# Optimization experiments

Measured on AMD Instinct MI355X. Metric: run time of the kernel, lower is better.

Reference implementation:

```python
import jax, jax.numpy as jnp
import numpy as np

V, D, E, K = 8192, 128, 262144, 512

def _sqrtm_psd(A):
    # symmetric PSD matrix square root via eigendecomposition
    w, v = jnp.linalg.eigh(A)
    w = jnp.clip(w, 0.0)
    return (v * jnp.sqrt(w)) @ v.T


def setup_inputs() -> dict:
    key = jax.random.key(0)
    k1, k2, k3, k4 = jax.random.split(key, 4)
    inputs = jax.random.normal(k1, (V, D), dtype=jnp.float32) * 0.1
    # targets must be SPD (it is passed through sqrtm as a covariance)
    A = jax.random.normal(k2, (K, K), dtype=jnp.float32) / np.sqrt(K)
    targets = A @ A.T + 0.1 * jnp.eye(K, dtype=jnp.float32)
    edge_index = jax.random.randint(k3, (2, E), 0, V, dtype=jnp.int32)
    pmat = jax.random.normal(k4, (K, V), dtype=jnp.float32) / np.sqrt(V)
    return {"inputs": inputs, "targets": targets, "edge_index": edge_index, "pmat": pmat}


def reference(inputs, targets, edge_index, pmat):
    n = inputs.shape[0]
    i, j = edge_index[0], edge_index[1]
    # per-edge squared distance -> exp weight (vectorized gather-compute)
    d = jnp.sum((inputs[i] - inputs[j]) ** 2, axis=-1)  # [E]
    w = jnp.exp(-d)
    # W starts as identity (self loops give exp(0)=1, same as eye); symmetric scatter
    W = jnp.eye(n, dtype=inputs.dtype)
    W = W.at[i, j].set(w).at[j, i].set(w)
    deg = W.sum(axis=1)
    L = jnp.diag(deg) - W
    k = pmat.shape[0]
    L_adj = pmat @ L @ pmat.T + 1e-05 * jnp.eye(k, dtype=inputs.dtype)
    S1 = jnp.linalg.inv(L_adj)
    S0 = targets.astype(jnp.float32)
    S0_sqrt = _sqrtm_psd(S0)
    S_ = _sqrtm_psd(S0_sqrt @ S1 @ S0_sqrt)
    return jnp.trace(S1) + jnp.trace(S0) - 2.0 * jnp.trace(S_)
```

## Files before the change

kernel.cpp:

```cpp
#include <hip/hip_runtime.h>
#include <math.h>

#define VN 8192
#define DN 128
#define EN 262144
#define KD 512
#define KK (KD*KD)

#define S_SS_LADJ 0
#define S_INV_C1  1
#define S_SS_S0   2
#define S_INV_C0  3
#define S_QRT_C0  4
#define S_SS_G    5
#define S_INV_CG  6
#define S_QRT_CG  7
#define S_TR_X    8
#define S_TR_S0   9
#define S_TR_YG   10

typedef __attribute__((ext_vector_type(8))) __bf16 bf16x8;
typedef __attribute__((ext_vector_type(4))) float f32x4;

static __device__ __forceinline__ float waveReduceAdd(float v) {
#pragma unroll
  for (int o = 32; o; o >>= 1) v += __shfl_xor(v, o);
  return v;
}

static __device__ __forceinline__ ushort f2b(float f) {
  unsigned x = __float_as_uint(f);
  unsigned r = (x + 0x7fffu + ((x >> 16) & 1u)) >> 16;
  return (ushort)r;
}
static __device__ __forceinline__ float b2f(ushort u) {
  return __uint_as_float((unsigned)u << 16);
}


__global__ __launch_bounds__(256) void transpose_k(const float* __restrict__ in,
                                                   float* __restrict__ out) {
  __shared__ float s[32][33];
  int tx = threadIdx.x & 31, ty = threadIdx.x >> 5;
  int v0 = blockIdx.x * 32, k0 = blockIdx.y * 32;
  for (int r = ty; r < 32; r += 8) s[r][tx] = in[(size_t)(k0 + r) * VN + v0 + tx];
  __syncthreads();
  for (int r = ty; r < 32; r += 8) out[(size_t)(v0 + r) * KD + k0 + tx] = s[tx][r];
}

__global__ __launch_bounds__(256) void count_k(const float* __restrict__ x,
                                               const int* __restrict__ ei,
                                               int* __restrict__ ea, int* __restrict__ eb,
                                               float* __restrict__ ew,
                                               int* __restrict__ cnt,
                                               unsigned int* __restrict__ bitmap) {
  int e = (int)(((unsigned)blockIdx.x * 256u + threadIdx.x) >> 6);
  int lane = threadIdx.x & 63;
  if (e >= EN) return;
  int i = ei[e], j = ei[EN + e];
  int a = i < j ? i : j;
  int b = i < j ? j : i;
  int ok = 0;
  if (lane == 0) {
    if (i != j) {
      unsigned key = (unsigned)a * (unsigned)VN + (unsigned)b;
      unsigned m = 1u << (key & 31u);
      unsigned old = atomicOr(bitmap + (key >> 5), m);
      ok = (old & m) ? 0 : 1;
    }
  }
  ok = __shfl(ok, 0);
  if (!ok) { if (lane == 0) ea[e] = -1; return; }
  float d0 = x[a * DN + lane]      - x[b * DN + lane];
  float d1 = x[a * DN + 64 + lane] - x[b * DN + 64 + lane];
  float s = d0 * d0 + d1 * d1;
  s = waveReduceAdd(s);
  if (lane == 0) {
    ea[e] = a; eb[e] = b; ew[e] = expf(-s);
    atomicAdd(cnt + a, 1);
    atomicAdd(cnt + b, 1);
  }
}

__global__ __launch_bounds__(1024) void scan_k(const int* __restrict__ cnt,
                                               int* __restrict__ rowptr,
                                               int* __restrict__ cursor) {
  __shared__ int sd[1024];
  __shared__ int carry;
  int tid = threadIdx.x;
  if (tid == 0) { carry = 0; rowptr[0] = 0; }
  __syncthreads();
  for (int c = 0; c < VN / 1024; ++c) {
    int v = c * 1024 + tid;
    int xv = cnt[v];
    sd[tid] = xv;
    __syncthreads();
    for (int off = 1; off < 1024; off <<= 1) {
      int t = (tid >= off) ? sd[tid - off] : 0;
      __syncthreads();
      sd[tid] += t;
      __syncthreads();
    }
    int incl = sd[tid];
    int base = carry;
    rowptr[v + 1] = base + incl;
    cursor[v] = base + incl - xv;
    __syncthreads();
    if (tid == 1023) carry = base + incl;
    __syncthreads();
  }
}

__global__ __launch_bounds__(256) void fill_k(const int* __restrict__ ea, const int* __restrict__ eb,
                                              const float* __restrict__ ew,
                                              int* __restrict__ cursor,
                                              int* __restrict__ adjj, float* __restrict__ adjw) {
  int e = blockIdx.x * 256 + threadIdx.x;
  if (e >= EN) return;
  int a = ea[e];
  if (a < 0) return;
  int b = eb[e];
  float w = ew[e];
  int p = atomicAdd(cursor + a, 1); adjj[p] = b; adjw[p] = w;
  int q = atomicAdd(cursor + b, 1); adjj[q] = a; adjw[q] = w;
}

__global__ __launch_bounds__(512) void buildB_k(const float* __restrict__ pmatT,
                                                const int* __restrict__ rowptr,
                                                const int* __restrict__ adjj,
                                                const float* __restrict__ adjw,
                                                float* __restrict__ Bout) {
  int v = blockIdx.x;
  int k = threadIdx.x;
  int s = rowptr[v], e = rowptr[v + 1];
  float a0 = 0.f, a1 = 0.f, a2 = 0.f, a3 = 0.f, sw = 0.f;
  int p = s;
  for (; p + 4 <= e; p += 4) {
    int j0 = adjj[p], j1 = adjj[p + 1], j2 = adjj[p + 2], j3 = adjj[p + 3];
    float w0 = adjw[p], w1 = adjw[p + 1], w2 = adjw[p + 2], w3 = adjw[p + 3];
    a0 += w0 * pmatT[(size_t)j0 * KD + k];
    a1 += w1 * pmatT[(size_t)j1 * KD + k];
    a2 += w2 * pmatT[(size_t)j2 * KD + k];
    a3 += w3 * pmatT[(size_t)j3 * KD + k];
    sw += w0 + w1 + w2 + w3;
  }
  for (; p < e; ++p) {
    int jj = adjj[p];
    float w = adjw[p];
    a0 += w * pmatT[(size_t)jj * KD + k];
    sw += w;
  }
  Bout[(size_t)v * KD + k] = sw * pmatT[(size_t)v * KD + k] - (a0 + a1 + a2 + a3);
}

__global__ __launch_bounds__(256) void gemm_big_k(const float* __restrict__ A,
                                                  const float* __restrict__ B,
                                                  float* __restrict__ C) {
  __shared__ __align__(16) float As[32][34];
  __shared__ __align__(16) float Bs[32][34];
  int tid = threadIdx.x;
  int tx = tid & 15, ty = tid >> 4;
  int n0 = blockIdx.x * 32, m0 = blockIdx.y * 32;
  int kbase = blockIdx.z * (VN / 8);
  float a00 = 0.f, a01 = 0.f, a10 = 0.f, a11 = 0.f;
  for (int kt = kbase; kt < kbase + VN / 8; kt += 32) {
#pragma unroll
    for (int u = 0; u < 4; ++u) {
      int li = tid * 4 + u;
      int r = li >> 5, c = li & 31;
      As[c][r] = A[(size_t)(m0 + r) * VN + kt + c];
      Bs[r][c] = B[(size_t)(kt + r) * KD + n0 + c];
    }
    __syncthreads();
#pragma unroll
    for (int k = 0; k < 32; ++k) {
      float2 av = *(const float2*)&As[k][2 * ty];
      float2 bv = *(const float2*)&Bs[k][2 * tx];
      a00 += av.x * bv.x; a01 += av.x * bv.y;
      a10 += av.y * bv.x; a11 += av.y * bv.y;
    }
    __syncthreads();
  }
  int m = m0 + 2 * ty, n = n0 + 2 * tx;
  atomicAdd(&C[m * KD + n], a00);
  atomicAdd(&C[m * KD + n + 1], a01);
  atomicAdd(&C[(m + 1) * KD + n], a10);
  atomicAdd(&C[(m + 1) * KD + n + 1], a11);
}


static __device__ __forceinline__ void g32_body(const float* __restrict__ A,
                                                const float* __restrict__ B,
                                                const float* __restrict__ Dm,
                                                float* __restrict__ C,
                                                float alpha, float beta) {
  __shared__ __align__(16) float As[32][34];
  __shared__ __align__(16) float Bs[32][34];
  int tid = threadIdx.x;
  int tx = tid & 15, ty = tid >> 4;
  int n0 = blockIdx.x * 32, m0 = blockIdx.y * 32;
  float a00 = 0.f, a01 = 0.f, a10 = 0.f, a11 = 0.f;
  for (int kt = 0; kt < KD; kt += 32) {
#pragma unroll
    for (int u = 0; u < 4; ++u) {
      int li = tid * 4 + u;
      int r = li >> 5, c = li & 31;
      As[c][r] = A[(m0 + r) * KD + kt + c];
      Bs[r][c] = B[(kt + r) * KD + n0 + c];
    }
    __syncthreads();
#pragma unroll
    for (int k = 0; k < 32; ++k) {
      float2 av = *(const float2*)&As[k][2 * ty];
      float2 bv = *(const float2*)&Bs[k][2 * tx];
      a00 += av.x * bv.x; a01 += av.x * bv.y;
      a10 += av.y * bv.x; a11 += av.y * bv.y;
    }
    __syncthreads();
  }
  int m = m0 + 2 * ty, n = n0 + 2 * tx;
  float d00 = 0.f, d01 = 0.f, d10 = 0.f, d11 = 0.f;
  if (beta != 0.0f) {
    d00 = Dm[m * KD + n];       d01 = Dm[m * KD + n + 1];
    d10 = Dm[(m + 1) * KD + n]; d11 = Dm[(m + 1) * KD + n + 1];
  }
  C[m * KD + n]           = alpha * a00 + beta * d00;
  C[m * KD + n + 1]       = alpha * a01 + beta * d01;
  C[(m + 1) * KD + n]     = alpha * a10 + beta * d10;
  C[(m + 1) * KD + n + 1] = alpha * a11 + beta * d11;
}

__global__ __launch_bounds__(256) void gemm_kk(const float* __restrict__ A,
                                               const float* __restrict__ B,
                                               const float* __restrict__ Dm,
                                               float* __restrict__ C,
                                               float alpha, float beta) {
  g32_body(A, B, Dm, C, alpha, beta);
}

__global__ __launch_bounds__(256) void gemm_dual32(const float* A0, const float* B0,
                                                   const float* D0, float* C0,
                                                   const float* A1, const float* B1,
                                                   const float* D1, float* C1,
                                                   float alpha, float beta) {
  if (blockIdx.z == 0) g32_body(A0, B0, D0, C0, alpha, beta);
  else                 g32_body(A1, B1, D1, C1, alpha, beta);
}


struct SmemT { ushort a[2][64][40]; ushort b[2][64][40]; };

static __device__ __forceinline__ void mgemm_s(SmemT* sm,
    const float* Asl, const float* Bsl, const float* Dsl, float* Csl,
    float alpha, float beta, int wsplit) {
  const ushort* Ah = (const ushort*)(Asl + KK);
  const ushort* Al = Ah + KK;
  const ushort* Bh = (const ushort*)(Bsl + KK);
  const ushort* Bl = Bh + KK;
  int tid = threadIdx.x;
  int lane = tid & 63, wave = tid >> 6;
  int wr = wave >> 1, wc = wave & 1;
  int fr = lane & 15, fq = lane >> 4;
  int m0 = blockIdx.y * 64, n0 = blockIdx.x * 64;
  int sr = tid >> 2, skc = (tid & 3) * 8;
  f32x4 acc[2][2] = {};
  for (int kt = 0; kt < KD; kt += 32) {
    *(uint4*)&sm->a[0][sr][skc] = *(const uint4*)&Ah[(size_t)(m0 + sr) * KD + kt + skc];
    *(uint4*)&sm->a[1][sr][skc] = *(const uint4*)&Al[(size_t)(m0 + sr) * KD + kt + skc];
    *(uint4*)&sm->b[0][sr][skc] = *(const uint4*)&Bh[(size_t)(n0 + sr) * KD + kt + skc];
    *(uint4*)&sm->b[1][sr][skc] = *(const uint4*)&Bl[(size_t)(n0 + sr) * KD + kt + skc];
    __syncthreads();
    bf16x8 ah[2], al[2], bh[2], bl[2];
#pragma unroll
    for (int m = 0; m < 2; ++m) {
      ah[m] = *(const bf16x8*)&sm->a[0][wr * 32 + m * 16 + fr][fq * 8];
      al[m] = *(const bf16x8*)&sm->a[1][wr * 32 + m * 16 + fr][fq * 8];
    }
#pragma unroll
    for (int n = 0; n < 2; ++n) {
      bh[n] = *(const bf16x8*)&sm->b[0][wc * 32 + n * 16 + fr][fq * 8];
      bl[n] = *(const bf16x8*)&sm->b[1][wc * 32 + n * 16 + fr][fq * 8];
    }
#pragma unroll
    for (int m = 0; m < 2; ++m)
#pragma unroll
      for (int n = 0; n < 2; ++n) {
        acc[m][n] = __builtin_amdgcn_mfma_f32_16x16x32_bf16(ah[m], bh[n], acc[m][n], 0, 0, 0);
        acc[m][n] = __builtin_amdgcn_mfma_f32_16x16x32_bf16(ah[m], bl[n], acc[m][n], 0, 0, 0);
        acc[m][n] = __builtin_amdgcn_mfma_f32_16x16x32_bf16(al[m], bh[n], acc[m][n], 0, 0, 0);
      }
    __syncthreads();
  }
  ushort* Ch = (ushort*)(Csl + KK);
  ushort* Cl = Ch + KK;
#pragma unroll
  for (int m = 0; m < 2; ++m)
#pragma unroll
    for (int n = 0; n < 2; ++n) {
      int col = n0 + wc * 32 + n * 16 + fr;
#pragma unroll
      for (int j = 0; j < 4; ++j) {
        int row = m0 + wr * 32 + m * 16 + fq * 4 + j;
        float v = alpha * acc[m][n][j];
        if (beta != 0.f) v += beta * Dsl[row * KD + col];
        Csl[row * KD + col] = v;
        if (wsplit) {
          ushort h = f2b(v);
          Ch[row * KD + col] = h;
          Cl[row * KD + col] = f2b(v - b2f(h));
        }
      }
    }
}

__global__ __launch_bounds__(256) void bc3_k(const float* Za, const float* Ya, float* Pm,
                                             const float* Xa, const float* Ra,
                                             float* Xb, float* Rb) {
  __shared__ SmemT sm;
  int z = blockIdx.z;
  if (z == 0)      mgemm_s(&sm, Za, Ya, nullptr, Pm, 1.f, 0.f, 1);
  else if (z == 1) mgemm_s(&sm, Xa, Ra, Xa, Xb, 1.f, 1.f, 1);
  else             mgemm_s(&sm, Ra, Ra, nullptr, Rb, 1.f, 0.f, 1);
}

__global__ __launch_bounds__(256) void yz2_k(const float* Ya, const float* Za, const float* Pm,
                                             float* Yb, float* Zb) {
  __shared__ SmemT sm;
  if (blockIdx.z == 0) mgemm_s(&sm, Ya, Pm, Ya, Yb, -0.5f, 1.5f, 1);
  else                 mgemm_s(&sm, Pm, Za, Za, Zb, -0.5f, 1.5f, 1);
}

__global__ __launch_bounds__(256) void pm1_k(const float* Za, const float* Ya, float* Pm) {
  __shared__ SmemT sm;
  mgemm_s(&sm, Za, Ya, nullptr, Pm, 1.f, 0.f, 1);
}


__global__ __launch_bounds__(256) void sumsq_k(const float* __restrict__ A, int n,
                                               float* __restrict__ slot) {
  float s = 0.f;
  for (int i = blockIdx.x * 256 + threadIdx.x; i < n; i += gridDim.x * 256) {
    float v = A[i];
    s += v * v;
  }
  __shared__ float p[4];
  s = waveReduceAdd(s);
  if ((threadIdx.x & 63) == 0) p[threadIdx.x >> 6] = s;
  __syncthreads();
  if (threadIdx.x == 0) atomicAdd(slot, p[0] + p[1] + p[2] + p[3]);
}

__global__ __launch_bounds__(512) void trace_k(const float* __restrict__ A,
                                               float* __restrict__ slot) {
  float v = A[(size_t)threadIdx.x * KD + threadIdx.x];
  __shared__ float p[8];
  v = waveReduceAdd(v);
  if ((threadIdx.x & 63) == 0) p[threadIdx.x >> 6] = v;
  __syncthreads();
  if (threadIdx.x == 0) {
    float t = 0.f;
    for (int i = 0; i < 8; ++i) t += p[i];
    slot[0] = t;
  }
}

__global__ void derive_k(const float* __restrict__ in, float* __restrict__ o_rsqrt,
                         float* __restrict__ o_qroot) {
  float x = in[0];
  o_rsqrt[0] = 1.0f / sqrtf(x);
  if (o_qroot) o_qroot[0] = powf(x, 0.25f);
}

__global__ __launch_bounds__(256) void setid_const_k(float* __restrict__ C, float val) {
  int idx = blockIdx.x * 256 + threadIdx.x;
  int r = idx >> 9, c = idx & (KD - 1);
  C[idx] = (r == c) ? val : 0.0f;
}

__global__ __launch_bounds__(256) void initinv_split_k(const float* __restrict__ Ladj,
                                                       const float* __restrict__ s,
                                                       float* __restrict__ X,
                                                       float* __restrict__ R) {
  int idx = blockIdx.x * 256 + threadIdx.x;
  int r = idx >> 9, c = idx & (KD - 1);
  float cv = s[0];
  float id = (r == c) ? 1.f : 0.f;
  float xv = id * cv;
  float rv = id - cv * Ladj[idx];
  ushort* Xh = (ushort*)(X + KK); ushort* Xl = Xh + KK;
  ushort* Rh = (ushort*)(R + KK); ushort* Rl = Rh + KK;
  X[idx] = xv; ushort h = f2b(xv); Xh[idx] = h; Xl[idx] = f2b(xv - b2f(h));
  R[idx] = rv; h = f2b(rv);        Rh[idx] = h; Rl[idx] = f2b(rv - b2f(h));
}

__global__ __launch_bounds__(256) void setid_split_k(float* __restrict__ C, float val) {
  int idx = blockIdx.x * 256 + threadIdx.x;
  int r = idx >> 9, c = idx & (KD - 1);
  float v = (r == c) ? val : 0.0f;
  ushort* Chh = (ushort*)(C + KK); ushort* Cll = Chh + KK;
  C[idx] = v; ushort h = f2b(v); Chh[idx] = h; Cll[idx] = f2b(v - b2f(h));
}

__global__ __launch_bounds__(256) void scale_split_k(const float* __restrict__ A,
                                                     const float* __restrict__ s,
                                                     float* __restrict__ C) {
  int idx = blockIdx.x * 256 + threadIdx.x;
  float v = A[idx] * s[0];
  ushort* Chh = (ushort*)(C + KK); ushort* Cll = Chh + KK;
  C[idx] = v; ushort h = f2b(v); Chh[idx] = h; Cll[idx] = f2b(v - b2f(h));
}

__global__ __launch_bounds__(256) void scale32_k(const float* __restrict__ A,
                                                 const float* __restrict__ s,
                                                 float* __restrict__ C) {
  int idx = blockIdx.x * 256 + threadIdx.x;
  C[idx] = A[idx] * s[0];
}

__global__ __launch_bounds__(256) void sym_k(const float* __restrict__ G,
                                             float* __restrict__ Out) {
  int idx = blockIdx.x * 256 + threadIdx.x;
  int r = idx >> 9, c = idx & (KD - 1);
  Out[idx] = 0.5f * (G[idx] + G[c * KD + r]);
}

__global__ void final_k(const float* __restrict__ scal, float* __restrict__ out) {
  out[0] = scal[S_TR_X] + scal[S_TR_S0] - 2.0f * scal[S_QRT_CG] * scal[S_TR_YG];
}


extern "C" void kernel_launch(void* const* d_in, const int* in_sizes, int n_in,
                              void* d_out, int out_size, void* d_ws, size_t ws_size,
                              hipStream_t stream) {
  (void)in_sizes; (void)n_in; (void)out_size; (void)ws_size;
  const float* x    = (const float*)d_in[0];
  const float* S0   = (const float*)d_in[1];
  const int*   ei   = (const int*)d_in[2];
  const float* pmat = (const float*)d_in[3];
  float* out = (float*)d_out;
  char* ws = (char*)d_ws;
  const size_t MB = 1u << 20;
  const size_t SLOT = 2 * MB;

  unsigned* bitmap = (unsigned*)ws;
  float* pmatT = (float*)(ws + 8 * MB);
  float* Bm    = (float*)(ws + 24 * MB);
  float* Ladj  = (float*)(ws + 40 * MB);
  float* Gs    = (float*)(ws + 41 * MB);
  int*   ea     = (int*)(ws + 40 * MB);
  int*   eb     = (int*)(ws + 41 * MB);
  float* ew     = (float*)(ws + 42 * MB);
  int*   adjj   = (int*)(ws + 43 * MB);
  float* adjw   = (float*)(ws + 45 * MB);
  int*   cnt    = (int*)(ws + 47 * MB);
  int*   rowptr = (int*)(ws + 47 * MB + 64 * 1024);
  int*   cursor = (int*)(ws + 47 * MB + 128 * 1024);
  float* scal   = (float*)(ws + 47 * MB + 256 * 1024);
  float* SL[11];
  for (int i = 0; i < 11; ++i) SL[i] = (float*)(ws + (size_t)i * SLOT);
  float *Xa = SL[0], *Ra = SL[1], *Ya = SL[2], *Za = SL[3];
  float *Xb = SL[4], *Rb = SL[5], *Yb = SL[6], *Zb = SL[7];
  float *Pm = SL[8], *S0h = SL[9], *TMP = SL[10];

  hipMemsetAsync(bitmap, 0, (size_t)VN * VN / 8, stream);
  hipMemsetAsync(cnt, 0, (size_t)VN * 4, stream);
  hipMemsetAsync(scal, 0, 64 * 4, stream);

  transpose_k<<<dim3(VN / 32, KD / 32), 256, 0, stream>>>(pmat, pmatT);
  count_k<<<EN / 4, 256, 0, stream>>>(x, ei, ea, eb, ew, cnt, bitmap);
  scan_k<<<1, 1024, 0, stream>>>(cnt, rowptr, cursor);
  fill_k<<<EN / 256, 256, 0, stream>>>(ea, eb, ew, cursor, adjj, adjw);
  buildB_k<<<VN, 512, 0, stream>>>(pmatT, rowptr, adjj, adjw, Bm);
  setid_const_k<<<KK / 256, 256, 0, stream>>>(Ladj, 1e-5f);
  gemm_big_k<<<dim3(16, 16, 8), 256, 0, stream>>>(pmat, Bm, Ladj);

  sumsq_k<<<256, 256, 0, stream>>>(Ladj, KK, &scal[S_SS_LADJ]);
  derive_k<<<1, 1, 0, stream>>>(&scal[S_SS_LADJ], &scal[S_INV_C1], nullptr);
  initinv_split_k<<<KK / 256, 256, 0, stream>>>(Ladj, &scal[S_INV_C1], Xa, Ra);

  sumsq_k<<<256, 256, 0, stream>>>(S0, KK, &scal[S_SS_S0]);
  derive_k<<<1, 1, 0, stream>>>(&scal[S_SS_S0], &scal[S_INV_C0], &scal[S_QRT_C0]);
  scale_split_k<<<KK / 256, 256, 0, stream>>>(S0, &scal[S_INV_C0], Ya);
  setid_split_k<<<KK / 256, 256, 0, stream>>>(Za, 1.0f);

  for (int r = 0; r < 15; ++r) {
    bc3_k<<<dim3(8, 8, 3), 256, 0, stream>>>(Za, Ya, Pm, Xa, Ra, Xb, Rb);
    yz2_k<<<dim3(8, 8, 2), 256, 0, stream>>>(Ya, Za, Pm, Yb, Zb);
    float* t = Xa; Xa = Xb; Xb = t;
    t = Ra; Ra = Rb; Rb = t;
    t = Ya; Ya = Yb; Yb = t;
    t = Za; Za = Zb; Zb = t;
  }

  float* U32  = Xb;
  float* Xfin = Rb;
  gemm_kk<<<dim3(16, 16), 256, 0, stream>>>(Ladj, Xa, nullptr, U32, 1.0f, 0.0f);
  gemm_kk<<<dim3(16, 16), 256, 0, stream>>>(Xa, U32, Xa, Xfin, -1.0f, 2.0f);
  trace_k<<<1, 512, 0, stream>>>(Xfin, &scal[S_TR_X]);
  trace_k<<<1, 512, 0, stream>>>(S0, &scal[S_TR_S0]);

  gemm_kk<<<dim3(16, 16), 256, 0, stream>>>(Za, Ya, nullptr, Pm, 1.0f, 0.0f);
  gemm_kk<<<dim3(16, 16), 256, 0, stream>>>(Ya, Pm, Ya, Yb, -0.5f, 1.5f);
  scale32_k<<<KK / 256, 256, 0, stream>>>(Yb, &scal[S_QRT_C0], S0h);

  gemm_kk<<<dim3(16, 16), 256, 0, stream>>>(S0h, Xfin, nullptr, TMP, 1.0f, 0.0f);
  gemm_kk<<<dim3(16, 16), 256, 0, stream>>>(TMP, S0h, nullptr, Gs, 1.0f, 0.0f);
  sym_k<<<KK / 256, 256, 0, stream>>>(Gs, TMP);
  sumsq_k<<<256, 256, 0, stream>>>(TMP, KK, &scal[S_SS_G]);
  derive_k<<<1, 1, 0, stream>>>(&scal[S_SS_G], &scal[S_INV_CG], &scal[S_QRT_CG]);
  scale_split_k<<<KK / 256, 256, 0, stream>>>(TMP, &scal[S_INV_CG], Ya);
  setid_split_k<<<KK / 256, 256, 0, stream>>>(Za, 1.0f);
  for (int r = 0; r < 20; ++r) {
    pm1_k<<<dim3(8, 8, 1), 256, 0, stream>>>(Za, Ya, Pm);
    yz2_k<<<dim3(8, 8, 2), 256, 0, stream>>>(Ya, Za, Pm, Yb, Zb);
    float* t = Ya; Ya = Yb; Yb = t;
    t = Za; Za = Zb; Zb = t;
  }
  gemm_kk<<<dim3(16, 16), 256, 0, stream>>>(Za, Ya, nullptr, Pm, 1.0f, 0.0f);
  gemm_dual32<<<dim3(16, 16, 2), 256, 0, stream>>>(Ya, Pm, Ya, Yb,
                                                   Pm, Za, Za, Zb, -0.5f, 1.5f);
  gemm_kk<<<dim3(16, 16), 256, 0, stream>>>(Zb, Yb, nullptr, Pm, 1.0f, 0.0f);
  gemm_kk<<<dim3(16, 16), 256, 0, stream>>>(Yb, Pm, Yb, S0h, -0.5f, 1.5f);
  trace_k<<<1, 512, 0, stream>>>(S0h, &scal[S_TR_YG]);

  final_k<<<1, 1, 0, stream>>>(scal, out);
}
```

Measured before the change: 1.580 ms.

## Vectorize edge distance, enlarge big GEMM tiles, batch tail GEMMs and traces

The edge kernel now uses 16 lanes per edge with float4 loads and a 16-lane shuffle reduction instead of a full wave per edge. The split-K projection GEMM moves from 32x32 to 64x64 output tiles with 4x4 register blocking, float4 loads and fewer atomics. Independent post-iteration GEMM pairs and the two trace reductions are merged into dual launches to cut kernel launch count. The cost is more registers in the GEMM and fewer blocks in flight.

New measurement: 1.466 ms. 7.2% less time.

```diff
diff --git a/kernel.cpp b/kernel.cpp
--- a/kernel.cpp
+++ b/kernel.cpp
@@ -54,14 +54,15 @@
                                                float* __restrict__ ew,
                                                int* __restrict__ cnt,
                                                unsigned int* __restrict__ bitmap) {
-  int e = (int)(((unsigned)blockIdx.x * 256u + threadIdx.x) >> 6);
+  int e = (int)(((unsigned)blockIdx.x * 256u + threadIdx.x) >> 4);
   int lane = threadIdx.x & 63;
+  int sl = lane & 15;
   if (e >= EN) return;
   int i = ei[e], j = ei[EN + e];
   int a = i < j ? i : j;
   int b = i < j ? j : i;
   int ok = 0;
-  if (lane == 0) {
+  if (sl == 0) {
     if (i != j) {
       unsigned key = (unsigned)a * (unsigned)VN + (unsigned)b;
       unsigned m = 1u << (key & 31u);
@@ -69,13 +70,17 @@
       ok = (old & m) ? 0 : 1;
     }
   }
-  ok = __shfl(ok, 0);
-  if (!ok) { if (lane == 0) ea[e] = -1; return; }
-  float d0 = x[a * DN + lane]      - x[b * DN + lane];
-  float d1 = x[a * DN + 64 + lane] - x[b * DN + 64 + lane];
-  float s = d0 * d0 + d1 * d1;
-  s = waveReduceAdd(s);
-  if (lane == 0) {
+  ok = __shfl(ok, lane & 48);
+  if (!ok) { if (sl == 0) ea[e] = -1; return; }
+  const float4* xa = (const float4*)&x[(size_t)a * DN + sl * 8];
+  const float4* xb = (const float4*)&x[(size_t)b * DN + sl * 8];
+  float4 a0 = xa[0], a1 = xa[1], b0 = xb[0], b1 = xb[1];
+  float d0 = a0.x - b0.x, d1 = a0.y - b0.y, d2 = a0.z - b0.z, d3 = a0.w - b0.w;
+  float d4 = a1.x - b1.x, d5 = a1.y - b1.y, d6 = a1.z - b1.z, d7 = a1.w - b1.w;
+  float s = d0*d0 + d1*d1 + d2*d2 + d3*d3 + d4*d4 + d5*d5 + d6*d6 + d7*d7;
+#pragma unroll
+  for (int o = 8; o; o >>= 1) s += __shfl_xor(s, o);
+  if (sl == 0) {
     ea[e] = a; eb[e] = b; ew[e] = expf(-s);
     atomicAdd(cnt + a, 1);
     atomicAdd(cnt + b, 1);
@@ -156,36 +161,42 @@
 __global__ __launch_bounds__(256) void gemm_big_k(const float* __restrict__ A,
                                                   const float* __restrict__ B,
                                                   float* __restrict__ C) {
-  __shared__ __align__(16) float As[32][34];
-  __shared__ __align__(16) float Bs[32][34];
+  __shared__ __align__(16) float As[32][68];
+  __shared__ __align__(16) float Bs[32][68];
   int tid = threadIdx.x;
   int tx = tid & 15, ty = tid >> 4;
-  int n0 = blockIdx.x * 32, m0 = blockIdx.y * 32;
+  int n0 = blockIdx.x * 64, m0 = blockIdx.y * 64;
   int kbase = blockIdx.z * (VN / 8);
-  float a00 = 0.f, a01 = 0.f, a10 = 0.f, a11 = 0.f;
+  float acc[4][4] = {};
   for (int kt = kbase; kt < kbase + VN / 8; kt += 32) {
 #pragma unroll
-    for (int u = 0; u < 4; ++u) {
-      int li = tid * 4 + u;
-      int r = li >> 5, c = li & 31;
-      As[c][r] = A[(size_t)(m0 + r) * VN + kt + c];
-      Bs[r][c] = B[(size_t)(kt + r) * KD + n0 + c];
+    for (int u = 0; u < 2; ++u) {
+      int li = tid * 2 + u;
+      int r = li >> 3, c = (li & 7) * 4;
+      float4 av = *(const float4*)&A[(size_t)(m0 + r) * VN + kt + c];
+      As[c][r] = av.x; As[c + 1][r] = av.y; As[c + 2][r] = av.z; As[c + 3][r] = av.w;
+      int rb = li >> 4, cb = (li & 15) * 4;
+      *(float4*)&Bs[rb][cb] = *(const float4*)&B[(size_t)(kt + rb) * KD + n0 + cb];
     }
     __syncthreads();
 #pragma unroll
     for (int k = 0; k < 32; ++k) {
-      float2 av = *(const float2*)&As[k][2 * ty];
-      float2 bv = *(const float2*)&Bs[k][2 * tx];
-      a00 += av.x * bv.x; a01 += av.x * bv.y;
-      a10 += av.y * bv.x; a11 += av.y * bv.y;
-    }
-    __syncthreads();
-  }
-  int m = m0 + 2 * ty, n = n0 + 2 * tx;
-  atomicAdd(&C[m * KD + n], a00);
-  atomicAdd(&C[m * KD + n + 1], a01);
-  atomicAdd(&C[(m + 1) * KD + n], a10);
-  atomicAdd(&C[(m + 1) * KD + n + 1], a11);
+      float4 av = *(const float4*)&As[k][ty * 4];
+      float4 bv = *(const float4*)&Bs[k][tx * 4];
+      float am[4] = {av.x, av.y, av.z, av.w};
+      float bm[4] = {bv.x, bv.y, bv.z, bv.w};
+#pragma unroll
+      for (int mi = 0; mi < 4; ++mi)
+#pragma unroll
+        for (int ni = 0; ni < 4; ++ni) acc[mi][ni] += am[mi] * bm[ni];
+    }
+    __syncthreads();
+  }
+#pragma unroll
+  for (int mi = 0; mi < 4; ++mi)
+#pragma unroll
+    for (int ni = 0; ni < 4; ++ni)
+      atomicAdd(&C[(m0 + ty * 4 + mi) * KD + n0 + tx * 4 + ni], acc[mi][ni]);
 }
 
 
@@ -240,11 +251,12 @@
 
 __global__ __launch_bounds__(256) void gemm_dual32(const float* A0, const float* B0,
                                                    const float* D0, float* C0,
+                                                   float alpha0, float beta0,
                                                    const float* A1, const float* B1,
                                                    const float* D1, float* C1,
-                                                   float alpha, float beta) {
-  if (blockIdx.z == 0) g32_body(A0, B0, D0, C0, alpha, beta);
-  else                 g32_body(A1, B1, D1, C1, alpha, beta);
+                                                   float alpha1, float beta1) {
+  if (blockIdx.z == 0) g32_body(A0, B0, D0, C0, alpha0, beta0);
+  else                 g32_body(A1, B1, D1, C1, alpha1, beta1);
 }
 
 
@@ -364,6 +376,22 @@
   }
 }
 
+__global__ __launch_bounds__(512) void trace2_k(const float* __restrict__ A0, float* s0,
+                                                const float* __restrict__ A1, float* s1) {
+  const float* A = blockIdx.z ? A1 : A0;
+  float* slot = blockIdx.z ? s1 : s0;
+  float v = A[(size_t)threadIdx.x * KD + threadIdx.x];
+  __shared__ float p[8];
+  v = waveReduceAdd(v);
+  if ((threadIdx.x & 63) == 0) p[threadIdx.x >> 6] = v;
+  __syncthreads();
+  if (threadIdx.x == 0) {
+    float t = 0.f;
+    for (int i = 0; i < 8; ++i) t += p[i];
+    slot[0] = t;
+  }
+}
+
 __global__ void derive_k(const float* __restrict__ in, float* __restrict__ o_rsqrt,
                          float* __restrict__ o_qroot) {
   float x = in[0];
@@ -467,12 +495,12 @@
   hipMemsetAsync(scal, 0, 64 * 4, stream);
 
   transpose_k<<<dim3(VN / 32, KD / 32), 256, 0, stream>>>(pmat, pmatT);
-  count_k<<<EN / 4, 256, 0, stream>>>(x, ei, ea, eb, ew, cnt, bitmap);
+  count_k<<<EN / 16, 256, 0, stream>>>(x, ei, ea, eb, ew, cnt, bitmap);
   scan_k<<<1, 1024, 0, stream>>>(cnt, rowptr, cursor);
   fill_k<<<EN / 256, 256, 0, stream>>>(ea, eb, ew, cursor, adjj, adjw);
   buildB_k<<<VN, 512, 0, stream>>>(pmatT, rowptr, adjj, adjw, Bm);
   setid_const_k<<<KK / 256, 256, 0, stream>>>(Ladj, 1e-5f);
-  gemm_big_k<<<dim3(16, 16, 8), 256, 0, stream>>>(pmat, Bm, Ladj);
+  gemm_big_k<<<dim3(8, 8, 8), 256, 0, stream>>>(pmat, Bm, Ladj);
 
   sumsq_k<<<256, 256, 0, stream>>>(Ladj, KK, &scal[S_SS_LADJ]);
   derive_k<<<1, 1, 0, stream>>>(&scal[S_SS_LADJ], &scal[S_INV_C1], nullptr);
@@ -494,13 +522,11 @@
 
   float* U32  = Xb;
   float* Xfin = Rb;
-  gemm_kk<<<dim3(16, 16), 256, 0, stream>>>(Ladj, Xa, nullptr, U32, 1.0f, 0.0f);
-  gemm_kk<<<dim3(16, 16), 256, 0, stream>>>(Xa, U32, Xa, Xfin, -1.0f, 2.0f);
-  trace_k<<<1, 512, 0, stream>>>(Xfin, &scal[S_TR_X]);
-  trace_k<<<1, 512, 0, stream>>>(S0, &scal[S_TR_S0]);
-
-  gemm_kk<<<dim3(16, 16), 256, 0, stream>>>(Za, Ya, nullptr, Pm, 1.0f, 0.0f);
-  gemm_kk<<<dim3(16, 16), 256, 0, stream>>>(Ya, Pm, Ya, Yb, -0.5f, 1.5f);
+  gemm_dual32<<<dim3(16, 16, 2), 256, 0, stream>>>(Ladj, Xa, nullptr, U32, 1.0f, 0.0f,
+                                                   Za, Ya, nullptr, Pm, 1.0f, 0.0f);
+  gemm_dual32<<<dim3(16, 16, 2), 256, 0, stream>>>(Xa, U32, Xa, Xfin, -1.0f, 2.0f,
+                                                   Ya, Pm, Ya, Yb, -0.5f, 1.5f);
+  trace2_k<<<dim3(1, 1, 2), 512, 0, stream>>>(Xfin, &scal[S_TR_X], S0, &scal[S_TR_S0]);
   scale32_k<<<KK / 256, 256, 0, stream>>>(Yb, &scal[S_QRT_C0], S0h);
 
   gemm_kk<<<dim3(16, 16), 256, 0, stream>>>(S0h, Xfin, nullptr, TMP, 1.0f, 0.0f);
@@ -517,7 +543,7 @@
     t = Za; Za = Zb; Zb = t;
   }
   gemm_kk<<<dim3(16, 16), 256, 0, stream>>>(Za, Ya, nullptr, Pm, 1.0f, 0.0f);
-  gemm_dual32<<<dim3(16, 16, 2), 256, 0, stream>>>(Ya, Pm, Ya, Yb,
+  gemm_dual32<<<dim3(16, 16, 2), 256, 0, stream>>>(Ya, Pm, Ya, Yb, -0.5f, 1.5f,
                                                    Pm, Za, Za, Zb, -0.5f, 1.5f);
   gemm_kk<<<dim3(16, 16), 256, 0, stream>>>(Zb, Yb, nullptr, Pm, 1.0f, 0.0f);
   gemm_kk<<<dim3(16, 16), 256, 0, stream>>>(Yb, Pm, Yb, S0h, -0.5f, 1.5f);
```
